# Kernel tuning notes

Measured on AMD Instinct MI355X. Metric: run time of the kernel, lower is better.

Reference implementation:

```python
import jax, jax.numpy as jnp
import numpy as np
import math

BATCH, SEQ_LEN, HIDDEN, STATE = 4, 2048, 1024, 64
N2 = STATE // 2  # complex modes
LOG_DT_MIN, LOG_DT_MAX = math.log(0.001), math.log(0.01)


def setup_inputs() -> dict:
    key = jax.random.key(0)
    ks = jax.random.split(key, 6)
    inp = jax.random.normal(ks[0], (BATCH, SEQ_LEN, HIDDEN), dtype=jnp.float32)
    log_dt = jax.random.uniform(ks[1], (HIDDEN,), dtype=jnp.float32) * (LOG_DT_MAX - LOG_DT_MIN) + LOG_DT_MIN
    D = jax.random.normal(ks[2], (HIDDEN,), dtype=jnp.float32)
    # s4d-lin init: A = 0.5 + i*pi*n, param stores log(real) and imag separately
    A_log = jnp.full((HIDDEN, N2), math.log(0.5), dtype=jnp.float32)
    A_imag = jnp.broadcast_to(math.pi * jnp.arange(N2, dtype=jnp.float32), (HIDDEN, N2)).copy()
    B = jax.random.normal(ks[3], (HIDDEN, N2, 2), dtype=jnp.float32)  # view_as_real of cfloat
    C = jax.random.normal(ks[4], (HIDDEN, N2, 2), dtype=jnp.float32)
    return {"input": inp, "log_dt": log_dt, "D": D, "A_log": A_log, "A_imag": A_imag, "B": B, "C": C}


def reference(input, log_dt, D, A_log, A_imag, B, C):
    dt = jnp.exp(log_dt)[:, None]                      # [H,1]
    A = -jnp.exp(A_log) + 1j * A_imag                  # [H,N2] complex, diagonal of diag_embed(A)
    # gbt (bilinear, alpha=0.5) on diagonal A:
    denom = 1.0 - dt / 2.0 * A
    A_disc = (1.0 + dt / 2.0 * A) / denom              # [H,N2]
    Bc = B[..., 0] + 1j * B[..., 1]                    # view_as_complex
    B_disc = dt * Bc / denom                           # [H,N2]
    Cc = (C[..., 0] + 1j * C[..., 1]) * 2.0            # [H,N2]

    x0 = jnp.zeros((input.shape[0], A_disc.shape[0], A_disc.shape[1]), dtype=A_disc.dtype)  # [B,H,N2]
    us = jnp.transpose(input, (1, 0, 2))               # [L,B,H]

    def step(x, u):
        # x_t = A x_{t-1} + B u_t (diagonal A => elementwise)
        x = A_disc * x + B_disc * u[:, :, None]
        y = jnp.einsum('hn,bhn->bh', Cc, x).real + D * u
        return x, y

    _, ys = jax.lax.scan(step, x0, us)                 # ys: [L,B,H]
    return jnp.transpose(ys, (1, 0, 2))                # [B,L,H]
```

## Files before the change

### kernel.cpp

```cpp
#include <hip/hip_runtime.h>
#include <math.h>

#define SEQLEN   2048
#define HIDDEN   1024
#define NMODES   32
#define CHANNELS 4096
#define CHB      16
#define TPG      1024
#define XP       72
#define CSTR     1032
#define XCH      (17 * XP)
#define SMEMN    (CHB * XCH)

typedef float  f2    __attribute__((ext_vector_type(2)));
typedef short  s8v   __attribute__((ext_vector_type(8)));
typedef float  f32x4 __attribute__((ext_vector_type(4)));
union Frag { s8v s; unsigned u[4]; };

#define SZ_V  (1024*64*64*2)
#define SZ_M  (1024*64*64*2)
#define SZ_K  (1024*64*4)
#define SZ_Q  (1024*64*4)
#define OFF_M (SZ_V)
#define OFF_K (OFF_M + SZ_M)
#define OFF_Q (OFF_K + SZ_K)
#define OFF_C (OFF_Q + SZ_Q)
#define SZ_C  (CHANNELS*64*4)
#define OFF_F (OFF_C + SZ_C)

template <int CTRL>
__device__ __forceinline__ float dpp_add(float p) {
    int t = __builtin_amdgcn_update_dpp(0, __float_as_int(p), CTRL, 0xF, 0xF, true);
    return p + __int_as_float(t);
}
template <int CTRL>
__device__ __forceinline__ float dpp_shr(float x) {
    int t = __builtin_amdgcn_update_dpp(0, __float_as_int(x), CTRL, 0xF, 0xF, true);
    return __int_as_float(t);
}
__device__ __forceinline__ float sum32_to16(float p) {
    p = dpp_add<0xB1>(p); p = dpp_add<0x4E>(p);
    p = dpp_add<0x124>(p); p = dpp_add<0x128>(p);
    p = dpp_add<0x142>(p);
    return p;
}
__device__ __forceinline__ unsigned cvt_pk_bf16(float lo, float hi) {
    unsigned d; asm("v_cvt_pk_bf16_f32 %0, %1, %2" : "=v"(d) : "v"(lo), "v"(hi)); return d;
}
__device__ __forceinline__ unsigned short bf16of(float x) {
    return (unsigned short)(cvt_pk_bf16(x, x) & 0xffffu);
}
__device__ __forceinline__ float bf2f(unsigned s) {
    return __uint_as_float(s << 16);
}

__device__ __forceinline__ void coef1(
    const float* __restrict__ log_dt, const float* __restrict__ A_log,
    const float* __restrict__ A_imag, const float* __restrict__ Bp,
    const float* __restrict__ Cp, int h, int m,
    float& adr, float& adi, float& bpr, float& bpi)
{
    const int idx = h * NMODES + m;
    const float dt = expf(log_dt[h]);
    const float hd = 0.5f * dt;
    const float ar = -expf(A_log[idx]);
    const float ai = A_imag[idx];
    const float dr = 1.f - hd * ar, di = -hd * ai;
    const float inv = 1.f / (dr * dr + di * di);
    const float nr = 1.f + hd * ar, ni = hd * ai;
    adr = (nr * dr + ni * di) * inv;
    adi = (ni * dr - nr * di) * inv;
    const float tbr = dt * Bp[idx * 2], tbi = dt * Bp[idx * 2 + 1];
    const float bdr = (tbr * dr + tbi * di) * inv;
    const float bdi = (tbi * dr - tbr * di) * inv;
    const float cr = 2.f * Cp[idx * 2], ci = 2.f * Cp[idx * 2 + 1];
    bpr = cr * bdr - ci * bdi;
    bpi = cr * bdi + ci * bdr;
}

__global__ __launch_bounds__(256) void ssm_tables(
    const float* __restrict__ log_dt, const float* __restrict__ Dp,
    const float* __restrict__ A_log, const float* __restrict__ A_imag,
    const float* __restrict__ Bp, const float* __restrict__ Cp,
    unsigned short* __restrict__ Vt, unsigned short* __restrict__ Mt,
    float* __restrict__ kct, float* __restrict__ Qt,
    int* __restrict__ flags)
{
    const int h = blockIdx.x >> 3, dg = blockIdx.x & 7;
    const int tid = threadIdx.x, wv = tid >> 6, l = tid & 63;
    const int m = l & 31;
    const int d = (dg * 4 + wv) * 2 + (l >> 5);

    if (blockIdx.x == 0) flags[tid] = 0;

    float adr, adi, bpr, bpi;
    coef1(log_dt, A_log, A_imag, Bp, Cp, h, m, adr, adi, bpr, bpi);

    float Pr = 1.f, Pi = 0.f, Qr = adr, Qi = adi;
    #pragma unroll
    for (int bit = 0; bit < 6; ++bit) {
        if ((d >> bit) & 1) { float t = Pr*Qr - Pi*Qi; Pi = Pr*Qi + Pi*Qr; Pr = t; }
        float tq = Qr*Qr - Qi*Qi; Qi = 2.f*Qr*Qi; Qr = tq;
    }
    const float wr  = Pr*bpr - Pi*bpi, wi  = Pr*bpi + Pi*bpr;
    const float apr = Pr*adr - Pi*adi, api = Pr*adi + Pi*adr;

    const size_t hb = (size_t)h * 64;
    Vt[(hb + m)      * 64 + (63 - d)] = bf16of(wr);
    Vt[(hb + 32 + m) * 64 + (63 - d)] = bf16of(wi);
    Mt[(hb + d) * 64 + m]       = bf16of(apr);
    Mt[(hb + d) * 64 + 32 + m]  = bf16of(-api);
    if (d == 63) {
        Qt[hb + m]      = apr;
        Qt[hb + 32 + m] = api;
    }

    float s = sum32_to16(wr);
    if ((l & 31) == 16) kct[hb + d] = s + (d == 0 ? Dp[h] : 0.f);
}

__device__ __forceinline__ void stage_frag_u(
    const float* __restrict__ ug, unsigned short* __restrict__ ubuf, int tid)
{
    #pragma unroll
    for (int it = 0; it < 16; ++it) {
        const int t_l = it * 64 + (tid >> 2);
        const int c4  = (tid & 3) * 4;
        const float4 g = *(const float4*)(ug + (size_t)t_l * HIDDEN + c4);
        const int n = t_l >> 6, rr = t_l & 63, ksw = rr >> 5, r5 = rr & 31;
        const int lane = (r5 >> 3) * 16 + n, j = r5 & 7;
        const int base = (ksw * 64 + lane) * 8 + j;
        ubuf[(c4 + 0) * CSTR + base] = bf16of(g.x);
        ubuf[(c4 + 1) * CSTR + base] = bf16of(g.y);
        ubuf[(c4 + 2) * CSTR + base] = bf16of(g.z);
        ubuf[(c4 + 3) * CSTR + base] = bf16of(g.w);
    }
    __syncthreads();
}

__global__ __launch_bounds__(256) void ssm_fused(
    const float* __restrict__ input,
    const unsigned short* __restrict__ Vt, const unsigned short* __restrict__ Mt,
    const float* __restrict__ kct, const float* __restrict__ Qt,
    float* __restrict__ carry, int* __restrict__ flags, float* __restrict__ out)
{
    __shared__ __align__(16) unsigned short smem[SMEMN];
    __shared__ float kcP[CHB][128];
    unsigned short* ubuf = smem;
    unsigned short* xb   = smem;

    const int tid = threadIdx.x, wv = tid >> 6, l = tid & 63;
    const int cgp = blockIdx.x >> 8;
    const int chb = blockIdx.x & 255;
    const int chbase = chb * CHB;
    const int b = chbase >> 10, h0 = chbase & (HIDDEN - 1);
    const int lr = l & 15, lk8 = ((l >> 4) & 3) * 8, lo = (l >> 4) * 4;

    #pragma unroll
    for (int q = 0; q < 8; ++q) {
        const int idx = q * 256 + tid, chl = idx >> 7, k = idx & 127;
        kcP[chl][k] = (k < 64) ? kct[(size_t)(h0 + chl) * 64 + (63 - k)] : 0.f;
    }
    stage_frag_u(input + ((size_t)b * SEQLEN + cgp * TPG) * HIDDEN + h0, ubuf, tid);

    Frag UBr[4][2];
    f32x4 acc_s[4][4];
    #pragma unroll
    for (int c = 0; c < 4; ++c) {
        const int chl = wv * 4 + c, h = h0 + chl;
        UBr[c][0].s = *(const s8v*)(ubuf + chl * CSTR + l * 8);
        UBr[c][1].s = *(const s8v*)(ubuf + chl * CSTR + (64 + l) * 8);
        #pragma unroll
        for (int mt = 0; mt < 4; ++mt) { f32x4 z = {0.f,0.f,0.f,0.f}; acc_s[c][mt] = z; }
        const unsigned short* Vh = Vt + (size_t)h * 4096;
        #pragma unroll
        for (int mt = 0; mt < 4; ++mt) {
            Frag VA0, VA1;
            VA0.s = *(const s8v*)(Vh + (16 * mt + lr) * 64 + lk8);
            VA1.s = *(const s8v*)(Vh + (16 * mt + lr) * 64 + 32 + lk8);
            acc_s[c][mt] = __builtin_amdgcn_mfma_f32_16x16x32_bf16(VA0.s, UBr[c][0].s, acc_s[c][mt], 0, 0, 0);
            acc_s[c][mt] = __builtin_amdgcn_mfma_f32_16x16x32_bf16(VA1.s, UBr[c][1].s, acc_s[c][mt], 0, 0, 0);
        }
    }
    __syncthreads();

    #pragma unroll
    for (int c = 0; c < 4; ++c) {
        const int chl = wv * 4 + c, ch = chbase + chl, h = h0 + chl;
        float QrA[4], QiA[4], QrB[4], QiB[4];
        {
            const float* qb = Qt + (size_t)h * 64;
            #pragma unroll
            for (int r = 0; r < 4; ++r) {
                QrA[r] = qb[lo + r];      QrB[r] = qb[16 + lo + r];
                QiA[r] = qb[32 + lo + r]; QiB[r] = qb[48 + lo + r];
            }
        }

        #define PSTEP(CTRL) { \
            float Y0[4], Y1[4], Y2[4], Y3[4]; \
            _Pragma("unroll") for (int r = 0; r < 4; ++r) { \
                Y0[r] = dpp_shr<CTRL>(acc_s[c][0][r]); Y1[r] = dpp_shr<CTRL>(acc_s[c][1][r]); \
                Y2[r] = dpp_shr<CTRL>(acc_s[c][2][r]); Y3[r] = dpp_shr<CTRL>(acc_s[c][3][r]); } \
            _Pragma("unroll") for (int r = 0; r < 4; ++r) { \
                acc_s[c][0][r] += QrA[r]*Y0[r] - QiA[r]*Y2[r]; \
                acc_s[c][2][r] += QrA[r]*Y2[r] + QiA[r]*Y0[r]; \
                acc_s[c][1][r] += QrB[r]*Y1[r] - QiB[r]*Y3[r]; \
                acc_s[c][3][r] += QrB[r]*Y3[r] + QiB[r]*Y1[r]; } }
        #define QSQ { _Pragma("unroll") for (int r = 0; r < 4; ++r) { \
            float tA = QrA[r]*QrA[r] - QiA[r]*QiA[r]; QiA[r] = 2.f*QrA[r]*QiA[r]; QrA[r] = tA; \
            float tB = QrB[r]*QrB[r] - QiB[r]*QiB[r]; QiB[r] = 2.f*QrB[r]*QiB[r]; QrB[r] = tB; } }
        PSTEP(0x111) QSQ
        PSTEP(0x112) QSQ
        PSTEP(0x114) QSQ
        PSTEP(0x118)
        #undef PSTEP
        #undef QSQ

        unsigned short* xc = xb + chl * XCH;
        #pragma unroll
        for (int mt = 0; mt < 4; ++mt) {
            *(unsigned*)(xc + (lr + 1) * XP + 16*mt + lo)     = cvt_pk_bf16(acc_s[c][mt][0], acc_s[c][mt][1]);
            *(unsigned*)(xc + (lr + 1) * XP + 16*mt + lo + 2) = cvt_pk_bf16(acc_s[c][mt][2], acc_s[c][mt][3]);
        }
        if (lr == 0) {
            #pragma unroll
            for (int g2 = 0; g2 < 4; ++g2) {
                *(unsigned*)(xc + 16*g2 + lo)     = 0u;
                *(unsigned*)(xc + 16*g2 + lo + 2) = 0u;
            }
        }
        if (cgp == 0 && lr == 15) {
            float* cb = carry + (size_t)ch * 64;
            #pragma unroll
            for (int r = 0; r < 4; ++r) {
                cb[lo + r]      = acc_s[c][0][r];
                cb[16 + lo + r] = acc_s[c][1][r];
                cb[32 + lo + r] = acc_s[c][2][r];
                cb[48 + lo + r] = acc_s[c][3][r];
            }
        }
    }

    if (cgp == 0) {
        __syncthreads();
        if (tid == 0) {
            __threadfence();
            __hip_atomic_store(&flags[chb], 1, __ATOMIC_RELEASE,
                               __HIP_MEMORY_SCOPE_AGENT);
        }
    }

    f32x4 acc[4][4];
    #pragma unroll
    for (int c = 0; c < 4; ++c) {
        const int chl = wv * 4 + c;
        #pragma unroll
        for (int mt = 0; mt < 4; ++mt) { f32x4 z = {0.f,0.f,0.f,0.f}; acc[c][mt] = z; }
        #pragma unroll
        for (int ks = 0; ks < 2; ++ks) {
            #pragma unroll
            for (int mt = 0; mt < 4; ++mt) {
                const int base = 63 - 16 * mt + 32 * ks + lk8 - lr;
                float f[8];
                #pragma unroll
                for (int j = 0; j < 8; ++j) f[j] = kcP[chl][base + j];
                Frag TA;
                #pragma unroll
                for (int q = 0; q < 4; ++q) TA.u[q] = cvt_pk_bf16(f[2*q], f[2*q+1]);
                acc[c][mt] = __builtin_amdgcn_mfma_f32_16x16x32_bf16(
                    TA.s, UBr[c][ks].s, acc[c][mt], 0, 0, 0);
            }
        }
    }

    if (cgp == 1) {
        if (tid == 0)
            while (__hip_atomic_load(&flags[chb], __ATOMIC_ACQUIRE,
                                     __HIP_MEMORY_SCOPE_AGENT) == 0)
                __builtin_amdgcn_s_sleep(2);
        __syncthreads();

        #pragma unroll
        for (int c = 0; c < 4; ++c) {
            const int chl = wv * 4 + c, ch = chbase + chl, h = h0 + chl;
            float PrA[4], PiA[4], PrB[4], PiB[4];
            {
                const float* qb = Qt + (size_t)h * 64;
                float QrA[4], QiA[4], QrB[4], QiB[4];
                #pragma unroll
                for (int r = 0; r < 4; ++r) {
                    QrA[r] = qb[lo + r];      QrB[r] = qb[16 + lo + r];
                    QiA[r] = qb[32 + lo + r]; QiB[r] = qb[48 + lo + r];
                    PrA[r] = 1.f; PiA[r] = 0.f; PrB[r] = 1.f; PiB[r] = 0.f;
                }
                #pragma unroll
                for (int bit = 0; bit < 4; ++bit) {
                    const bool on = (lr >> bit) & 1;
                    #pragma unroll
                    for (int r = 0; r < 4; ++r) {
                        const float nAr = PrA[r]*QrA[r] - PiA[r]*QiA[r];
                        const float nAi = PrA[r]*QiA[r] + PiA[r]*QrA[r];
                        const float nBr = PrB[r]*QrB[r] - PiB[r]*QiB[r];
                        const float nBi = PrB[r]*QiB[r] + PiB[r]*QrB[r];
                        PrA[r] = on ? nAr : PrA[r]; PiA[r] = on ? nAi : PiA[r];
                        PrB[r] = on ? nBr : PrB[r]; PiB[r] = on ? nBi : PiB[r];
                        const float sAr = QrA[r]*QrA[r] - QiA[r]*QiA[r];
                        QiA[r] = 2.f*QrA[r]*QiA[r]; QrA[r] = sAr;
                        const float sBr = QrB[r]*QrB[r] - QiB[r]*QiB[r];
                        QiB[r] = 2.f*QrB[r]*QiB[r]; QrB[r] = sBr;
                    }
                }
            }
            const float* cb = carry + (size_t)ch * 64;
            float aR[4], aI[4], bR[4], bI[4];
            #pragma unroll
            for (int r = 0; r < 4; ++r) {
                const float CrA = cb[lo + r],      CrB = cb[16 + lo + r];
                const float CiA = cb[32 + lo + r], CiB = cb[48 + lo + r];
                aR[r] = PrA[r]*CrA - PiA[r]*CiA;
                aI[r] = PrA[r]*CiA + PiA[r]*CrA;
                bR[r] = PrB[r]*CrB - PiB[r]*CiB;
                bI[r] = PrB[r]*CiB + PiB[r]*CrB;
            }
            const float* segs[4] = { aR, bR, aI, bI };
            unsigned short* xc = xb + chl * XCH;
            #pragma unroll
            for (int g2 = 0; g2 < 4; ++g2) {
                unsigned short* p = xc + lr * XP + 16*g2 + lo;
                const unsigned w0 = *(unsigned*)p;
                const unsigned w1 = *(unsigned*)(p + 2);
                const float f0 = bf2f(w0 & 0xffffu) + segs[g2][0];
                const float f1 = bf2f(w0 >> 16)     + segs[g2][1];
                const float f2 = bf2f(w1 & 0xffffu) + segs[g2][2];
                const float f3 = bf2f(w1 >> 16)     + segs[g2][3];
                *(unsigned*)p       = cvt_pk_bf16(f0, f1);
                *(unsigned*)(p + 2) = cvt_pk_bf16(f2, f3);
            }
        }
    }

    __syncthreads();

    #pragma unroll
    for (int c = 0; c < 4; ++c) {
        const int chl = wv * 4 + c, h = h0 + chl;
        const unsigned short* xc = xb + chl * XCH;
        Frag XB[2];
        XB[0].s = *(const s8v*)(xc + lr * XP + lk8);
        XB[1].s = *(const s8v*)(xc + lr * XP + 32 + lk8);
        const unsigned short* Mh = Mt + (size_t)h * 4096;
        #pragma unroll
        for (int ks = 0; ks < 2; ++ks) {
            #pragma unroll
            for (int mt = 0; mt < 4; ++mt) {
                Frag MA; MA.s = *(const s8v*)(Mh + (16 * mt + lr) * 64 + ks * 32 + lk8);
                acc[c][mt] = __builtin_amdgcn_mfma_f32_16x16x32_bf16(
                    MA.s, XB[ks].s, acc[c][mt], 0, 0, 0);
            }
        }
    }

    float* ob = out + ((size_t)b * SEQLEN + cgp * TPG) * HIDDEN + h0;
    #pragma unroll
    for (int half = 0; half < 2; ++half) {
        __syncthreads();
        if ((lr >> 3) == half) {
            const int lr7 = lr & 7;
            #pragma unroll
            for (int c = 0; c < 4; ++c) {
                const int chl = wv * 4 + c;
                const int col = chl ^ (lr7 << 1);
                #pragma unroll
                for (int mt = 0; mt < 4; ++mt)
                    #pragma unroll
                    for (int r = 0; r < 4; ++r) {
                        const int t_loc = lr7 * 64 + 16 * mt + lo + r;
                        smem[t_loc * 32 + col] = bf16of(acc[c][mt][r]);
                    }
            }
        }
        __syncthreads();
        float* obh = ob + (size_t)half * 512 * HIDDEN;
        #pragma unroll
        for (int q = 0; q < 8; ++q) {
            const int idx = q * 256 + tid;
            const int t_loc = idx >> 2, a = idx & 3;
            const int lrt = (t_loc >> 6) & 7;
            const int blk = (a ^ (lrt >> 1)) * 4;
            const uint2 w = *(const uint2*)(smem + t_loc * 32 + blk);
            const float s0 = bf2f(w.x & 0xffffu), s1 = bf2f(w.x >> 16);
            const float s2 = bf2f(w.y & 0xffffu), s3 = bf2f(w.y >> 16);
            float4 o;
            if (lrt & 1) o = make_float4(s2, s3, s0, s1);
            else         o = make_float4(s0, s1, s2, s3);
            *(float4*)(obh + (size_t)t_loc * HIDDEN + a * 4) = o;
        }
    }
}

extern "C" void kernel_launch(void* const* d_in, const int* in_sizes, int n_in,
                              void* d_out, int out_size, void* d_ws, size_t ws_size,
                              hipStream_t stream) {
    const float* input  = (const float*)d_in[0];
    const float* log_dt = (const float*)d_in[1];
    const float* Dp     = (const float*)d_in[2];
    const float* A_log  = (const float*)d_in[3];
    const float* A_imag = (const float*)d_in[4];
    const float* Bp     = (const float*)d_in[5];
    const float* Cp     = (const float*)d_in[6];
    float* out = (float*)d_out;

    unsigned short* Vt  = (unsigned short*)d_ws;
    unsigned short* Mtb = (unsigned short*)((char*)d_ws + OFF_M);
    float*          kct = (float*)((char*)d_ws + OFF_K);
    float*          Qt  = (float*)((char*)d_ws + OFF_Q);
    float*          carry = (float*)((char*)d_ws + OFF_C);
    int*            flags = (int*)((char*)d_ws + OFF_F);

    ssm_tables<<<dim3(1024 * 8), dim3(256), 0, stream>>>(
        log_dt, Dp, A_log, A_imag, Bp, Cp, Vt, Mtb, kct, Qt, flags);
    ssm_fused<<<dim3(512), dim3(256), 0, stream>>>(
        input, Vt, Mtb, kct, Qt, carry, flags, out);
}
```

Baseline: 66.87 us.

## Halve channels per block to double grid size and rework output staging

Cuts the channels handled by each fused block from 16 to 8, so each wave processes 2 channels instead of 4 and the grid doubles to 1024 blocks. The flag array and its indexing are extended to cover both channel halves. The output writeback is rebuilt as a single pass that packs two channels per 32-bit LDS store with an XOR swizzle, replacing the two-half staging. The aim is better occupancy and CU coverage on a chip with many CUs, at the cost of writing shorter contiguous rows per block (8 floats) and more blocks doing the spin-wait handoff.

```diff
diff --git a/kernel.cpp b/kernel.cpp
--- a/kernel.cpp
+++ b/kernel.cpp
@@ -5,7 +5,7 @@
 #define HIDDEN   1024
 #define NMODES   32
 #define CHANNELS 4096
-#define CHB      16
+#define CHB      8
 #define TPG      1024
 #define XP       72
 #define CSTR     1032
@@ -91,7 +91,7 @@
     const int m = l & 31;
     const int d = (dg * 4 + wv) * 2 + (l >> 5);
 
-    if (blockIdx.x == 0) flags[tid] = 0;
+    if (blockIdx.x == 0) { flags[tid] = 0; flags[256 + tid] = 0; }
 
     float adr, adi, bpr, bpi;
     coef1(log_dt, A_log, A_imag, Bp, Cp, h, m, adr, adi, bpr, bpi);
@@ -123,9 +123,9 @@
     const float* __restrict__ ug, unsigned short* __restrict__ ubuf, int tid)
 {
     #pragma unroll
-    for (int it = 0; it < 16; ++it) {
-        const int t_l = it * 64 + (tid >> 2);
-        const int c4  = (tid & 3) * 4;
+    for (int it = 0; it < 8; ++it) {
+        const int t_l = it * 128 + (tid >> 1);
+        const int c4  = (tid & 1) * 4;
         const float4 g = *(const float4*)(ug + (size_t)t_l * HIDDEN + c4);
         const int n = t_l >> 6, rr = t_l & 63, ksw = rr >> 5, r5 = rr & 31;
         const int lane = (r5 >> 3) * 16 + n, j = r5 & 7;
@@ -150,24 +150,27 @@
     unsigned short* xb   = smem;
 
     const int tid = threadIdx.x, wv = tid >> 6, l = tid & 63;
-    const int cgp = blockIdx.x >> 8;
-    const int chb = blockIdx.x & 255;
-    const int chbase = chb * CHB;
+    const int p   = blockIdx.x & 511;
+    const int sH  = blockIdx.x >> 9;
+    const int cgp = p >> 8;
+    const int chb = p & 255;
+    const int fidx = sH * 256 + chb;
+    const int chbase = chb * 16 + sH * 8;
     const int b = chbase >> 10, h0 = chbase & (HIDDEN - 1);
     const int lr = l & 15, lk8 = ((l >> 4) & 3) * 8, lo = (l >> 4) * 4;
 
     #pragma unroll
-    for (int q = 0; q < 8; ++q) {
+    for (int q = 0; q < 4; ++q) {
         const int idx = q * 256 + tid, chl = idx >> 7, k = idx & 127;
         kcP[chl][k] = (k < 64) ? kct[(size_t)(h0 + chl) * 64 + (63 - k)] : 0.f;
     }
     stage_frag_u(input + ((size_t)b * SEQLEN + cgp * TPG) * HIDDEN + h0, ubuf, tid);
 
-    Frag UBr[4][2];
-    f32x4 acc_s[4][4];
-    #pragma unroll
-    for (int c = 0; c < 4; ++c) {
-        const int chl = wv * 4 + c, h = h0 + chl;
+    Frag UBr[2][2];
+    f32x4 acc_s[2][4];
+    #pragma unroll
+    for (int c = 0; c < 2; ++c) {
+        const int chl = wv * 2 + c, h = h0 + chl;
         UBr[c][0].s = *(const s8v*)(ubuf + chl * CSTR + l * 8);
         UBr[c][1].s = *(const s8v*)(ubuf + chl * CSTR + (64 + l) * 8);
         #pragma unroll
@@ -185,8 +188,8 @@
     __syncthreads();
 
     #pragma unroll
-    for (int c = 0; c < 4; ++c) {
-        const int chl = wv * 4 + c, ch = chbase + chl, h = h0 + chl;
+    for (int c = 0; c < 2; ++c) {
+        const int chl = wv * 2 + c, ch = chbase + chl, h = h0 + chl;
         float QrA[4], QiA[4], QrB[4], QiB[4];
         {
             const float* qb = Qt + (size_t)h * 64;
@@ -246,15 +249,15 @@
         __syncthreads();
         if (tid == 0) {
             __threadfence();
-            __hip_atomic_store(&flags[chb], 1, __ATOMIC_RELEASE,
+            __hip_atomic_store(&flags[fidx], 1, __ATOMIC_RELEASE,
                                __HIP_MEMORY_SCOPE_AGENT);
         }
     }
 
-    f32x4 acc[4][4];
-    #pragma unroll
-    for (int c = 0; c < 4; ++c) {
-        const int chl = wv * 4 + c;
+    f32x4 acc[2][4];
+    #pragma unroll
+    for (int c = 0; c < 2; ++c) {
+        const int chl = wv * 2 + c;
         #pragma unroll
         for (int mt = 0; mt < 4; ++mt) { f32x4 z = {0.f,0.f,0.f,0.f}; acc[c][mt] = z; }
         #pragma unroll
@@ -276,14 +279,14 @@
 
     if (cgp == 1) {
         if (tid == 0)
-            while (__hip_atomic_load(&flags[chb], __ATOMIC_ACQUIRE,
+            while (__hip_atomic_load(&flags[fidx], __ATOMIC_ACQUIRE,
                                      __HIP_MEMORY_SCOPE_AGENT) == 0)
                 __builtin_amdgcn_s_sleep(2);
         __syncthreads();
 
         #pragma unroll
-        for (int c = 0; c < 4; ++c) {
-            const int chl = wv * 4 + c, ch = chbase + chl, h = h0 + chl;
+        for (int c = 0; c < 2; ++c) {
+            const int chl = wv * 2 + c, ch = chbase + chl, h = h0 + chl;
             float PrA[4], PiA[4], PrB[4], PiB[4];
             {
                 const float* qb = Qt + (size_t)h * 64;
@@ -327,15 +330,15 @@
             unsigned short* xc = xb + chl * XCH;
             #pragma unroll
             for (int g2 = 0; g2 < 4; ++g2) {
-                unsigned short* p = xc + lr * XP + 16*g2 + lo;
-                const unsigned w0 = *(unsigned*)p;
-                const unsigned w1 = *(unsigned*)(p + 2);
+                unsigned short* pp = xc + lr * XP + 16*g2 + lo;
+                const unsigned w0 = *(unsigned*)pp;
+                const unsigned w1 = *(unsigned*)(pp + 2);
                 const float f0 = bf2f(w0 & 0xffffu) + segs[g2][0];
                 const float f1 = bf2f(w0 >> 16)     + segs[g2][1];
                 const float f2 = bf2f(w1 & 0xffffu) + segs[g2][2];
                 const float f3 = bf2f(w1 >> 16)     + segs[g2][3];
-                *(unsigned*)p       = cvt_pk_bf16(f0, f1);
-                *(unsigned*)(p + 2) = cvt_pk_bf16(f2, f3);
+                *(unsigned*)pp       = cvt_pk_bf16(f0, f1);
+                *(unsigned*)(pp + 2) = cvt_pk_bf16(f2, f3);
             }
         }
     }
@@ -343,8 +346,8 @@
     __syncthreads();
 
     #pragma unroll
-    for (int c = 0; c < 4; ++c) {
-        const int chl = wv * 4 + c, h = h0 + chl;
+    for (int c = 0; c < 2; ++c) {
+        const int chl = wv * 2 + c, h = h0 + chl;
         const unsigned short* xc = xb + chl * XCH;
         Frag XB[2];
         XB[0].s = *(const s8v*)(xc + lr * XP + lk8);
@@ -361,41 +364,30 @@
         }
     }
 
-    float* ob = out + ((size_t)b * SEQLEN + cgp * TPG) * HIDDEN + h0;
-    #pragma unroll
-    for (int half = 0; half < 2; ++half) {
-        __syncthreads();
-        if ((lr >> 3) == half) {
-            const int lr7 = lr & 7;
-            #pragma unroll
-            for (int c = 0; c < 4; ++c) {
-                const int chl = wv * 4 + c;
-                const int col = chl ^ (lr7 << 1);
-                #pragma unroll
-                for (int mt = 0; mt < 4; ++mt)
-                    #pragma unroll
-                    for (int r = 0; r < 4; ++r) {
-                        const int t_loc = lr7 * 64 + 16 * mt + lo + r;
-                        smem[t_loc * 32 + col] = bf16of(acc[c][mt][r]);
-                    }
-            }
-        }
-        __syncthreads();
-        float* obh = ob + (size_t)half * 512 * HIDDEN;
-        #pragma unroll
-        for (int q = 0; q < 8; ++q) {
-            const int idx = q * 256 + tid;
-            const int t_loc = idx >> 2, a = idx & 3;
-            const int lrt = (t_loc >> 6) & 7;
-            const int blk = (a ^ (lrt >> 1)) * 4;
-            const uint2 w = *(const uint2*)(smem + t_loc * 32 + blk);
-            const float s0 = bf2f(w.x & 0xffffu), s1 = bf2f(w.x >> 16);
-            const float s2 = bf2f(w.y & 0xffffu), s3 = bf2f(w.y >> 16);
-            float4 o;
-            if (lrt & 1) o = make_float4(s2, s3, s0, s1);
-            else         o = make_float4(s0, s1, s2, s3);
-            *(float4*)(obh + (size_t)t_loc * HIDDEN + a * 4) = o;
-        }
+    __syncthreads();
+
+    #pragma unroll
+    for (int mt = 0; mt < 4; ++mt)
+        #pragma unroll
+        for (int r = 0; r < 4; ++r) {
+            const int t_loc = lr * 64 + 16 * mt + lo + r;
+            const int colp  = wv ^ (lr & 3);
+            *(unsigned*)&smem[t_loc * 8 + colp * 2] =
+                cvt_pk_bf16(acc[0][mt][r], acc[1][mt][r]);
+        }
+    __syncthreads();
+
+    float* obh = out + ((size_t)b * SEQLEN + cgp * TPG) * HIDDEN + h0;
+    #pragma unroll
+    for (int q = 0; q < 8; ++q) {
+        const int idx = q * 256 + tid;
+        const int t_loc = idx >> 1, h4 = idx & 1;
+        const int sN = (t_loc >> 6) & 3;
+        const unsigned w0 = *(const unsigned*)&smem[t_loc * 8 + ((h4 * 2)     ^ sN) * 2];
+        const unsigned w1 = *(const unsigned*)&smem[t_loc * 8 + ((h4 * 2 + 1) ^ sN) * 2];
+        float4 o = make_float4(bf2f(w0 & 0xffffu), bf2f(w0 >> 16),
+                               bf2f(w1 & 0xffffu), bf2f(w1 >> 16));
+        *(float4*)(obh + (size_t)t_loc * HIDDEN + h4 * 4) = o;
     }
 }
 
@@ -420,6 +412,6 @@
 
     ssm_tables<<<dim3(1024 * 8), dim3(256), 0, stream>>>(
         log_dt, Dp, A_log, A_imag, Bp, Cp, Vt, Mtb, kct, Qt, flags);
-    ssm_fused<<<dim3(512), dim3(256), 0, stream>>>(
+    ssm_fused<<<dim3(1024), dim3(256), 0, stream>>>(
         input, Vt, Mtb, kct, Qt, carry, flags, out);
 }
```

Measured after the change: 89.02 us. 1.33x slower.
